# Optimization experiments

Measured on AMD Instinct MI355X. Metric: run time of the kernel, lower is better.

## Reference

```python
import jax, jax.numpy as jnp
import numpy as np

D_MODEL = 1024
NUM_HEADS = 16
HEAD_DIM = D_MODEL // NUM_HEADS


def setup_inputs() -> dict:
    key = jax.random.key(0)
    ks = jax.random.split(key, 11)
    B, S = 2, 2048
    s = 1.0 / np.sqrt(D_MODEL)
    return {
        "q": jax.random.normal(ks[0], (B, S, D_MODEL), jnp.float32),
        "k": jax.random.normal(ks[1], (B, S, D_MODEL), jnp.float32),
        "v": jax.random.normal(ks[2], (B, S, D_MODEL), jnp.float32),
        "Wq": jax.random.normal(ks[3], (D_MODEL, D_MODEL), jnp.float32) * s,
        "bq": jnp.zeros((D_MODEL,), jnp.float32),
        "Wk": jax.random.normal(ks[4], (D_MODEL, D_MODEL), jnp.float32) * s,
        "bk": jnp.zeros((D_MODEL,), jnp.float32),
        "Wv": jax.random.normal(ks[5], (D_MODEL, D_MODEL), jnp.float32) * s,
        "bv": jnp.zeros((D_MODEL,), jnp.float32),
        "Wo": jax.random.normal(ks[6], (D_MODEL, D_MODEL), jnp.float32) * s,
        "bo": jnp.zeros((D_MODEL,), jnp.float32),
    }


def _split_heads(x):
    B, S, _ = x.shape
    return x.reshape(B, S, NUM_HEADS, HEAD_DIM).transpose(0, 2, 1, 3)  # [B,H,S,Dh]


def reference(q, k, v, Wq, bq, Wk, bk, Wv, bv, Wo, bo):
    B, S, _ = q.shape
    qh = _split_heads(q @ Wq.T + bq)
    kh = _split_heads(k @ Wk.T + bk)
    vh = _split_heads(v @ Wv.T + bv)
    scale = 1.0 / jnp.sqrt(jnp.asarray(HEAD_DIM, qh.dtype))
    scores = jnp.einsum("bhqd,bhkd->bhqk", qh, kh) * scale  # [B,H,S,S]
    attn = jax.nn.softmax(scores, axis=-1)
    out = jnp.einsum("bhqk,bhkd->bhqd", attn, vh)
    out = out.transpose(0, 2, 1, 3).reshape(B, S, D_MODEL)
    return out @ Wo.T + bo
```

## Files before the change

### kernel.cpp

```cpp
#include <hip/hip_runtime.h>
#include <cstdint>
#include <cstddef>

#define DEVI __device__ __forceinline__

typedef short bf16x8 __attribute__((ext_vector_type(8)));
typedef float f32x4 __attribute__((ext_vector_type(4)));
typedef unsigned short u16x4 __attribute__((ext_vector_type(4)));

constexpr int D_MODEL = 1024;
constexpr int HEADS = 16;
constexpr int DH = 64;
constexpr int SEQ = 2048;
constexpr int KDIM = 1024;

DEVI unsigned short f2bf(float f) {
  union { float f; unsigned u; } v; v.f = f;
  unsigned r = v.u + 0x7fffu + ((v.u >> 16) & 1u);
  return (unsigned short)(r >> 16);
}

DEVI void cp16(const void* g, void* l) {
  __builtin_amdgcn_global_load_lds(
      (const __attribute__((address_space(1))) void*)g,
      (__attribute__((address_space(3))) void*)l, 16, 0, 0);
}

__global__ void __launch_bounds__(256) castall(
    const float* __restrict__ q, const float* __restrict__ k, const float* __restrict__ v,
    const float* __restrict__ Wq, const float* __restrict__ Wk,
    const float* __restrict__ Wv, const float* __restrict__ Wo,
    unsigned short* __restrict__ qb, unsigned short* __restrict__ kb, unsigned short* __restrict__ vb,
    unsigned short* __restrict__ Wqb, unsigned short* __restrict__ Wkb,
    unsigned short* __restrict__ Wvb, unsigned short* __restrict__ Wob) {
  int bid = blockIdx.x;
  const float* s; unsigned short* d; int off;
  if (bid < 12288) {
    int w = bid >> 12; off = bid & 4095;
    s = (w == 0) ? q : ((w == 1) ? k : v);
    d = (w == 0) ? qb : ((w == 1) ? kb : vb);
  } else {
    int w = (bid - 12288) >> 10; off = bid & 1023;
    s = (w == 0) ? Wq : ((w == 1) ? Wk : ((w == 2) ? Wv : Wo));
    d = (w == 0) ? Wqb : ((w == 1) ? Wkb : ((w == 2) ? Wvb : Wob));
  }
  int i = (off * 256 + threadIdx.x) * 4;
  float4 x = *(const float4*)(s + i);
  u16x4 o; o[0] = f2bf(x.x); o[1] = f2bf(x.y); o[2] = f2bf(x.z); o[3] = f2bf(x.w);
  *(u16x4*)(d + i) = o;
}

DEVI void gemm_body(const unsigned short* __restrict__ A, const unsigned short* __restrict__ W,
                    const float* __restrict__ bias, unsigned short* __restrict__ obf,
                    float* __restrict__ of32, float oscale, int mode, int bm, int bn,
                    unsigned short* As, unsigned short* Bs) {
  const int tid = threadIdx.x, lane = tid & 63, wave = tid >> 6;
  const int l16 = lane & 15, quad = lane >> 4;
  const int wm = (wave >> 1) * 64, wn = (wave & 1) * 64;
  const int sw = (l16 >> 1) & 3;
  f32x4 acc[4][4] = {};

  for (int k0 = 0; k0 < KDIM; k0 += 32) {
#pragma unroll
    for (int c = 0; c < 2; ++c) {
      int slot = c * 256 + tid;
      int row = slot >> 2, pblk = slot & 3;
      int col = (pblk ^ ((row >> 1) & 3)) * 8;
      cp16(A + (size_t)(bm * 128 + row) * KDIM + k0 + col, &As[slot * 8]);
      cp16(W + (size_t)(bn * 128 + row) * KDIM + k0 + col, &Bs[slot * 8]);
    }
    asm volatile("s_waitcnt vmcnt(0)" ::: "memory");
    __syncthreads();
    bf16x8 af[4], bfr[4];
#pragma unroll
    for (int t = 0; t < 4; ++t)
      af[t] = *(const bf16x8*)&As[(wm + t * 16 + l16) * 32 + ((quad ^ sw) * 8)];
#pragma unroll
    for (int t = 0; t < 4; ++t)
      bfr[t] = *(const bf16x8*)&Bs[(wn + t * 16 + l16) * 32 + ((quad ^ sw) * 8)];
#pragma unroll
    for (int i = 0; i < 4; ++i)
#pragma unroll
      for (int j = 0; j < 4; ++j)
        acc[i][j] = __builtin_amdgcn_mfma_f32_16x16x32_bf16(af[i], bfr[j], acc[i][j], 0, 0, 0);
    __syncthreads();
  }

#pragma unroll
  for (int i = 0; i < 4; ++i) {
#pragma unroll
    for (int j = 0; j < 4; ++j) {
      const int col = bn * 128 + wn + j * 16 + l16;
      const float bv = bias[col];
#pragma unroll
      for (int r = 0; r < 4; ++r) {
        const int row = bm * 128 + wm + i * 16 + quad * 4 + r;
        const float val = (acc[i][j][r] + bv) * oscale;
        if (mode == 2) {
          of32[(size_t)row * D_MODEL + col] = val;
        } else {
          const int b = row >> 11, s = row & (SEQ - 1);
          const int h = col >> 6, d = col & (DH - 1);
          size_t idx;
          if (mode == 0) idx = ((size_t)(b * HEADS + h) * SEQ + s) * DH + d;
          else           idx = ((size_t)(b * HEADS + h) * DH + d) * SEQ + s;
          obf[idx] = f2bf(val);
        }
      }
    }
  }
}

__global__ void __launch_bounds__(256) qkv_gemm(
    const unsigned short* __restrict__ qb, const unsigned short* __restrict__ kb,
    const unsigned short* __restrict__ vb,
    const unsigned short* __restrict__ Wqb, const unsigned short* __restrict__ Wkb,
    const unsigned short* __restrict__ Wvb,
    const float* __restrict__ bq, const float* __restrict__ bk, const float* __restrict__ bv,
    unsigned short* __restrict__ Qh, unsigned short* __restrict__ Kh,
    unsigned short* __restrict__ Vt, float qscale) {
  __shared__ unsigned short As[128 * 32], Bs[128 * 32];
  const int bid = blockIdx.x, seg = bid >> 8, inner = bid & 255;
  const int bm = inner >> 3, bn = inner & 7;
  const unsigned short* A = (seg == 0) ? qb : ((seg == 1) ? kb : vb);
  const unsigned short* W = (seg == 0) ? Wqb : ((seg == 1) ? Wkb : Wvb);
  const float* bias = (seg == 0) ? bq : ((seg == 1) ? bk : bv);
  unsigned short* O = (seg == 0) ? Qh : ((seg == 1) ? Kh : Vt);
  gemm_body(A, W, bias, O, nullptr, (seg == 0) ? qscale : 1.0f, (seg == 2) ? 1 : 0, bm, bn, As, Bs);
}

__global__ void __launch_bounds__(256) out_gemm(const unsigned short* __restrict__ AO,
                                                const unsigned short* __restrict__ Wob,
                                                const float* __restrict__ bo,
                                                float* __restrict__ out) {
  __shared__ unsigned short As[128 * 32], Bs[128 * 32];
  const int bid = blockIdx.x, bm = bid >> 3, bn = bid & 7;
  gemm_body(AO, Wob, bo, nullptr, out, 1.0f, 2, bm, bn, As, Bs);
}

__global__ void __launch_bounds__(256) attn(const unsigned short* __restrict__ Qh,
                                            const unsigned short* __restrict__ Kh,
                                            const unsigned short* __restrict__ Vt,
                                            unsigned short* __restrict__ AO) {
  __shared__ unsigned short Ks[2 * 64 * 64];
  __shared__ unsigned short Vs[2 * 64 * 64];
  __shared__ unsigned short Ps[4][16 * 64];
  const int bid = blockIdx.x;
  const int qt = bid >> 5, head = bid & 31, b = head >> 4, h = head & 15;
  const int tid = threadIdx.x;
  const int lane = tid & 63, wave = tid >> 6;
  const int l16 = lane & 15, quad = lane >> 4;
  const int sw7 = l16 & 7;

  const unsigned short* Qhead = Qh + (size_t)(b * HEADS + h) * SEQ * DH;
  const unsigned short* Khead = Kh + (size_t)(b * HEADS + h) * SEQ * DH;
  const unsigned short* Vhead = Vt + (size_t)(b * HEADS + h) * DH * SEQ;

  const int qrow = qt * 64 + wave * 16 + l16;
  bf16x8 aq0 = *(const bf16x8*)&Qhead[(size_t)qrow * DH + quad * 8];
  bf16x8 aq1 = *(const bf16x8*)&Qhead[(size_t)qrow * DH + 32 + quad * 8];

  const short onev = (l16 == 0) ? (short)0x3F80 : (short)0;
  bf16x8 bone = {onev, onev, onev, onev, onev, onev, onev, onev};

  f32x4 o[4] = {};
  f32x4 ol = {};

  for (int kc = 0; kc < SEQ / 128; ++kc) {
    const unsigned short* Kc = Khead + (size_t)kc * 128 * DH;
#pragma unroll
    for (int c = 0; c < 4; ++c) {
      int slot = c * 256 + tid;
      int row = slot >> 3;
      int jb = (slot & 7) ^ (row & 7);
      cp16(Kc + (size_t)row * DH + jb * 8, &Ks[slot * 8]);
      int sub = slot >> 9, s512 = slot & 511;
      int d = s512 >> 3;
      int jv = (s512 & 7) ^ (d & 7);
      cp16(Vhead + (size_t)d * SEQ + kc * 128 + sub * 64 + jv * 8, &Vs[slot * 8]);
    }
    asm volatile("s_waitcnt vmcnt(0)" ::: "memory");
    __syncthreads();

#pragma unroll
    for (int sub = 0; sub < 2; ++sub) {
      const unsigned short* K64 = &Ks[sub * 4096];
      const unsigned short* V64 = &Vs[sub * 4096];

      f32x4 st[4];
#pragma unroll
      for (int kt = 0; kt < 4; ++kt) {
        const int krow = kt * 16 + l16;
        bf16x8 bk0 = *(const bf16x8*)&K64[krow * 64 + ((quad ^ sw7) * 8)];
        bf16x8 bk1 = *(const bf16x8*)&K64[krow * 64 + (((quad + 4) ^ sw7) * 8)];
        f32x4 z = {};
        z = __builtin_amdgcn_mfma_f32_16x16x32_bf16(aq0, bk0, z, 0, 0, 0);
        z = __builtin_amdgcn_mfma_f32_16x16x32_bf16(aq1, bk1, z, 0, 0, 0);
        st[kt] = z;
      }

#pragma unroll
      for (int kt = 0; kt < 4; ++kt) {
        const int lb = kt * 2 + (l16 >> 3);
#pragma unroll
        for (int r = 0; r < 4; ++r) {
          const int rr = quad * 4 + r;
          float p = __builtin_amdgcn_exp2f(st[kt][r]);
          Ps[wave][rr * 64 + ((lb ^ (rr & 7)) << 3) + (l16 & 7)] =
              (unsigned short)(__float_as_uint(p) >> 16);
        }
      }
      asm volatile("s_waitcnt lgkmcnt(0)" ::: "memory");

      bf16x8 ap0 = *(const bf16x8*)&Ps[wave][l16 * 64 + ((quad ^ sw7) << 3)];
      bf16x8 ap1 = *(const bf16x8*)&Ps[wave][l16 * 64 + (((quad + 4) ^ sw7) << 3)];
#pragma unroll
      for (int nt = 0; nt < 4; ++nt) {
        const int vrow = nt * 16 + l16;
        bf16x8 bv0 = *(const bf16x8*)&V64[vrow * 64 + ((quad ^ sw7) * 8)];
        bf16x8 bv1 = *(const bf16x8*)&V64[vrow * 64 + (((quad + 4) ^ sw7) * 8)];
        o[nt] = __builtin_amdgcn_mfma_f32_16x16x32_bf16(ap0, bv0, o[nt], 0, 0, 0);
        o[nt] = __builtin_amdgcn_mfma_f32_16x16x32_bf16(ap1, bv1, o[nt], 0, 0, 0);
      }
      ol = __builtin_amdgcn_mfma_f32_16x16x32_bf16(ap0, bone, ol, 0, 0, 0);
      ol = __builtin_amdgcn_mfma_f32_16x16x32_bf16(ap1, bone, ol, 0, 0, 0);
    }
    __syncthreads();
  }

  float linv[4];
#pragma unroll
  for (int r = 0; r < 4; ++r) {
    float l = __shfl(ol[r], 0, 16);
    linv[r] = 1.0f / l;
  }
#pragma unroll
  for (int nt = 0; nt < 4; ++nt)
#pragma unroll
    for (int r = 0; r < 4; ++r) {
      const int qq = qt * 64 + wave * 16 + quad * 4 + r;
      AO[((size_t)(b * SEQ + qq)) * D_MODEL + h * 64 + nt * 16 + l16] =
          f2bf(o[nt][r] * linv[r]);
    }
}

extern "C" void kernel_launch(void* const* d_in, const int* in_sizes, int n_in,
                              void* d_out, int out_size, void* d_ws, size_t ws_size,
                              hipStream_t stream) {
  const float* q  = (const float*)d_in[0];
  const float* k  = (const float*)d_in[1];
  const float* v  = (const float*)d_in[2];
  const float* Wq = (const float*)d_in[3];
  const float* bq = (const float*)d_in[4];
  const float* Wk = (const float*)d_in[5];
  const float* bk = (const float*)d_in[6];
  const float* Wv = (const float*)d_in[7];
  const float* bv = (const float*)d_in[8];
  const float* Wo = (const float*)d_in[9];
  const float* bo = (const float*)d_in[10];
  float* out = (float*)d_out;

  char* ws = (char*)d_ws;
  const size_t MB = 1ull << 20;
  unsigned short* qb  = (unsigned short*)(ws + 0 * MB);
  unsigned short* kb  = (unsigned short*)(ws + 8 * MB);
  unsigned short* vb  = (unsigned short*)(ws + 16 * MB);
  unsigned short* Wqb = (unsigned short*)(ws + 24 * MB);
  unsigned short* Wkb = (unsigned short*)(ws + 26 * MB);
  unsigned short* Wvb = (unsigned short*)(ws + 28 * MB);
  unsigned short* Wob = (unsigned short*)(ws + 30 * MB);
  unsigned short* Qh  = (unsigned short*)(ws + 32 * MB);
  unsigned short* Kh  = (unsigned short*)(ws + 40 * MB);
  unsigned short* Vt  = (unsigned short*)(ws + 48 * MB);
  unsigned short* AO  = (unsigned short*)(ws + 56 * MB);

  castall<<<16384, 256, 0, stream>>>(q, k, v, Wq, Wk, Wv, Wo,
                                     qb, kb, vb, Wqb, Wkb, Wvb, Wob);

  const float qscale = 0.125f * 1.44269504088896f;
  qkv_gemm<<<768, 256, 0, stream>>>(qb, kb, vb, Wqb, Wkb, Wvb, bq, bk, bv,
                                    Qh, Kh, Vt, qscale);

  attn<<<1024, 256, 0, stream>>>(Qh, Kh, Vt, AO);

  out_gemm<<<256, 256, 0, stream>>>(AO, Wob, bo, out);
}
```

Before: 244.2 us.

## Use 32x32 MFMA register-resident attention and 64-row GEMM tiles

The attention kernel is rebuilt around 32x32 MFMA tiles. Scores are computed transposed so the exponentiated probabilities stay in registers as the B operand of the PV product, which removes the per-wave LDS round trip for P. The row sum is kept as a scalar instead of an extra MFMA, and the two key-split waves are reduced through LDS with a coalesced epilogue store. The projection GEMMs also move from 128x128 to 64x128 tiles, doubling the grid to raise occupancy at the cost of more reloads of the weight tiles.

```diff
diff --git a/kernel.cpp b/kernel.cpp
--- a/kernel.cpp
+++ b/kernel.cpp
@@ -5,7 +5,9 @@
 #define DEVI __device__ __forceinline__
 
 typedef short bf16x8 __attribute__((ext_vector_type(8)));
+typedef short bf16x4 __attribute__((ext_vector_type(4)));
 typedef float f32x4 __attribute__((ext_vector_type(4)));
+typedef float f32x16 __attribute__((ext_vector_type(16)));
 typedef unsigned short u16x4 __attribute__((ext_vector_type(4)));
 
 constexpr int D_MODEL = 1024;
@@ -20,10 +22,23 @@
   return (unsigned short)(r >> 16);
 }
 
+DEVI unsigned pkbf(float a, float b) {
+  return __builtin_amdgcn_perm(__float_as_uint(b), __float_as_uint(a), 0x07060302u);
+}
+
 DEVI void cp16(const void* g, void* l) {
   __builtin_amdgcn_global_load_lds(
       (const __attribute__((address_space(1))) void*)g,
       (__attribute__((address_space(3))) void*)l, 16, 0, 0);
+}
+
+DEVI f32x16 mfma_32x32x8(bf16x4 a, bf16x4 b, f32x16 c) {
+#if __has_builtin(__builtin_amdgcn_mfma_f32_32x32x8bf16_1k)
+  return __builtin_amdgcn_mfma_f32_32x32x8bf16_1k(a, b, c, 0, 0, 0);
+#else
+  asm volatile("v_mfma_f32_32x32x8_bf16 %0, %1, %2, %0" : "+v"(c) : "v"(a), "v"(b));
+  return c;
+#endif
 }
 
 __global__ void __launch_bounds__(256) castall(
@@ -50,38 +65,42 @@
   *(u16x4*)(d + i) = o;
 }
 
-DEVI void gemm_body(const unsigned short* __restrict__ A, const unsigned short* __restrict__ W,
-                    const float* __restrict__ bias, unsigned short* __restrict__ obf,
-                    float* __restrict__ of32, float oscale, int mode, int bm, int bn,
-                    unsigned short* As, unsigned short* Bs) {
+DEVI void gemm_body64(const unsigned short* __restrict__ A, const unsigned short* __restrict__ W,
+                      const float* __restrict__ bias, unsigned short* __restrict__ obf,
+                      float* __restrict__ of32, float oscale, int mode, int bm, int bn,
+                      unsigned short* As, unsigned short* Bs) {
   const int tid = threadIdx.x, lane = tid & 63, wave = tid >> 6;
   const int l16 = lane & 15, quad = lane >> 4;
-  const int wm = (wave >> 1) * 64, wn = (wave & 1) * 64;
+  const int wn = wave * 32;
   const int sw = (l16 >> 1) & 3;
-  f32x4 acc[4][4] = {};
+  f32x4 acc[4][2] = {};
 
   for (int k0 = 0; k0 < KDIM; k0 += 32) {
+    {
+      int row = tid >> 2, pblk = tid & 3;
+      int col = (pblk ^ ((row >> 1) & 3)) * 8;
+      cp16(A + (size_t)(bm * 64 + row) * KDIM + k0 + col, &As[tid * 8]);
+    }
 #pragma unroll
     for (int c = 0; c < 2; ++c) {
       int slot = c * 256 + tid;
       int row = slot >> 2, pblk = slot & 3;
       int col = (pblk ^ ((row >> 1) & 3)) * 8;
-      cp16(A + (size_t)(bm * 128 + row) * KDIM + k0 + col, &As[slot * 8]);
       cp16(W + (size_t)(bn * 128 + row) * KDIM + k0 + col, &Bs[slot * 8]);
     }
     asm volatile("s_waitcnt vmcnt(0)" ::: "memory");
     __syncthreads();
-    bf16x8 af[4], bfr[4];
+    bf16x8 af[4], bfr[2];
 #pragma unroll
     for (int t = 0; t < 4; ++t)
-      af[t] = *(const bf16x8*)&As[(wm + t * 16 + l16) * 32 + ((quad ^ sw) * 8)];
-#pragma unroll
-    for (int t = 0; t < 4; ++t)
-      bfr[t] = *(const bf16x8*)&Bs[(wn + t * 16 + l16) * 32 + ((quad ^ sw) * 8)];
+      af[t] = *(const bf16x8*)&As[(t * 16 + l16) * 32 + ((quad ^ sw) * 8)];
+#pragma unroll
+    for (int u = 0; u < 2; ++u)
+      bfr[u] = *(const bf16x8*)&Bs[(wn + u * 16 + l16) * 32 + ((quad ^ sw) * 8)];
 #pragma unroll
     for (int i = 0; i < 4; ++i)
 #pragma unroll
-      for (int j = 0; j < 4; ++j)
+      for (int j = 0; j < 2; ++j)
         acc[i][j] = __builtin_amdgcn_mfma_f32_16x16x32_bf16(af[i], bfr[j], acc[i][j], 0, 0, 0);
     __syncthreads();
   }
@@ -89,12 +108,12 @@
 #pragma unroll
   for (int i = 0; i < 4; ++i) {
 #pragma unroll
-    for (int j = 0; j < 4; ++j) {
+    for (int j = 0; j < 2; ++j) {
       const int col = bn * 128 + wn + j * 16 + l16;
       const float bv = bias[col];
 #pragma unroll
       for (int r = 0; r < 4; ++r) {
-        const int row = bm * 128 + wm + i * 16 + quad * 4 + r;
+        const int row = bm * 64 + i * 16 + quad * 4 + r;
         const float val = (acc[i][j][r] + bv) * oscale;
         if (mode == 2) {
           of32[(size_t)row * D_MODEL + col] = val;
@@ -119,129 +138,157 @@
     const float* __restrict__ bq, const float* __restrict__ bk, const float* __restrict__ bv,
     unsigned short* __restrict__ Qh, unsigned short* __restrict__ Kh,
     unsigned short* __restrict__ Vt, float qscale) {
-  __shared__ unsigned short As[128 * 32], Bs[128 * 32];
-  const int bid = blockIdx.x, seg = bid >> 8, inner = bid & 255;
+  __shared__ unsigned short As[64 * 32], Bs[128 * 32];
+  const int bid = blockIdx.x, seg = bid >> 9, inner = bid & 511;
   const int bm = inner >> 3, bn = inner & 7;
   const unsigned short* A = (seg == 0) ? qb : ((seg == 1) ? kb : vb);
   const unsigned short* W = (seg == 0) ? Wqb : ((seg == 1) ? Wkb : Wvb);
   const float* bias = (seg == 0) ? bq : ((seg == 1) ? bk : bv);
   unsigned short* O = (seg == 0) ? Qh : ((seg == 1) ? Kh : Vt);
-  gemm_body(A, W, bias, O, nullptr, (seg == 0) ? qscale : 1.0f, (seg == 2) ? 1 : 0, bm, bn, As, Bs);
+  gemm_body64(A, W, bias, O, nullptr, (seg == 0) ? qscale : 1.0f, (seg == 2) ? 1 : 0, bm, bn, As, Bs);
 }
 
 __global__ void __launch_bounds__(256) out_gemm(const unsigned short* __restrict__ AO,
                                                 const unsigned short* __restrict__ Wob,
                                                 const float* __restrict__ bo,
                                                 float* __restrict__ out) {
-  __shared__ unsigned short As[128 * 32], Bs[128 * 32];
+  __shared__ unsigned short As[64 * 32], Bs[128 * 32];
   const int bid = blockIdx.x, bm = bid >> 3, bn = bid & 7;
-  gemm_body(AO, Wob, bo, nullptr, out, 1.0f, 2, bm, bn, As, Bs);
+  gemm_body64(AO, Wob, bo, nullptr, out, 1.0f, 2, bm, bn, As, Bs);
 }
 
 __global__ void __launch_bounds__(256) attn(const unsigned short* __restrict__ Qh,
                                             const unsigned short* __restrict__ Kh,
                                             const unsigned short* __restrict__ Vt,
                                             unsigned short* __restrict__ AO) {
-  __shared__ unsigned short Ks[2 * 64 * 64];
-  __shared__ unsigned short Vs[2 * 64 * 64];
-  __shared__ unsigned short Ps[4][16 * 64];
+  __shared__ __align__(16) char smem[32768];
+  unsigned short* Ks = (unsigned short*)smem;
+  unsigned short* Vs = (unsigned short*)(smem + 16384);
+
   const int bid = blockIdx.x;
   const int qt = bid >> 5, head = bid & 31, b = head >> 4, h = head & 15;
   const int tid = threadIdx.x;
   const int lane = tid & 63, wave = tid >> 6;
-  const int l16 = lane & 15, quad = lane >> 4;
-  const int sw7 = l16 & 7;
+  const int wq = wave >> 1, wk = wave & 1;
+  const int l31 = lane & 31, hh = lane >> 5;
 
   const unsigned short* Qhead = Qh + (size_t)(b * HEADS + h) * SEQ * DH;
   const unsigned short* Khead = Kh + (size_t)(b * HEADS + h) * SEQ * DH;
   const unsigned short* Vhead = Vt + (size_t)(b * HEADS + h) * DH * SEQ;
 
-  const int qrow = qt * 64 + wave * 16 + l16;
-  bf16x8 aq0 = *(const bf16x8*)&Qhead[(size_t)qrow * DH + quad * 8];
-  bf16x8 aq1 = *(const bf16x8*)&Qhead[(size_t)qrow * DH + 32 + quad * 8];
-
-  const short onev = (l16 == 0) ? (short)0x3F80 : (short)0;
-  bf16x8 bone = {onev, onev, onev, onev, onev, onev, onev, onev};
-
-  f32x4 o[4] = {};
-  f32x4 ol = {};
+  const int qrow = qt * 64 + wq * 32 + l31;
+  bf16x8 aq[4];
+#pragma unroll
+  for (int it = 0; it < 4; ++it)
+    aq[it] = *(const bf16x8*)&Qhead[(size_t)qrow * DH + it * 16 + hh * 8];
+
+  f32x16 oacc[2] = {};
+  float lsum = 0.f;
 
   for (int kc = 0; kc < SEQ / 128; ++kc) {
-    const unsigned short* Kc = Khead + (size_t)kc * 128 * DH;
 #pragma unroll
     for (int c = 0; c < 4; ++c) {
-      int slot = c * 256 + tid;
-      int row = slot >> 3;
-      int jb = (slot & 7) ^ (row & 7);
-      cp16(Kc + (size_t)row * DH + jb * 8, &Ks[slot * 8]);
-      int sub = slot >> 9, s512 = slot & 511;
-      int d = s512 >> 3;
-      int jv = (s512 & 7) ^ (d & 7);
-      cp16(Vhead + (size_t)d * SEQ + kc * 128 + sub * 64 + jv * 8, &Vs[slot * 8]);
+      int s = c * 256 + tid;
+      int row = s >> 3, pblk = s & 7;
+      int jb = pblk ^ (row & 7);
+      cp16(Khead + (size_t)(kc * 128 + row) * DH + jb * 8, &Ks[s * 8]);
+    }
+#pragma unroll
+    for (int c = 0; c < 4; ++c) {
+      int s = c * 256 + tid;
+      int d = s >> 4, pblk = s & 15;
+      int jb = pblk ^ (d & 7);
+      cp16(Vhead + (size_t)d * SEQ + kc * 128 + jb * 8, &Vs[s * 8]);
     }
     asm volatile("s_waitcnt vmcnt(0)" ::: "memory");
     __syncthreads();
 
 #pragma unroll
     for (int sub = 0; sub < 2; ++sub) {
-      const unsigned short* K64 = &Ks[sub * 4096];
-      const unsigned short* V64 = &Vs[sub * 4096];
-
-      f32x4 st[4];
-#pragma unroll
-      for (int kt = 0; kt < 4; ++kt) {
-        const int krow = kt * 16 + l16;
-        bf16x8 bk0 = *(const bf16x8*)&K64[krow * 64 + ((quad ^ sw7) * 8)];
-        bf16x8 bk1 = *(const bf16x8*)&K64[krow * 64 + (((quad + 4) ^ sw7) * 8)];
-        f32x4 z = {};
-        z = __builtin_amdgcn_mfma_f32_16x16x32_bf16(aq0, bk0, z, 0, 0, 0);
-        z = __builtin_amdgcn_mfma_f32_16x16x32_bf16(aq1, bk1, z, 0, 0, 0);
-        st[kt] = z;
-      }
-
-#pragma unroll
-      for (int kt = 0; kt < 4; ++kt) {
-        const int lb = kt * 2 + (l16 >> 3);
-#pragma unroll
-        for (int r = 0; r < 4; ++r) {
-          const int rr = quad * 4 + r;
-          float p = __builtin_amdgcn_exp2f(st[kt][r]);
-          Ps[wave][rr * 64 + ((lb ^ (rr & 7)) << 3) + (l16 & 7)] =
-              (unsigned short)(__float_as_uint(p) >> 16);
+      const int kb32 = sub * 64 + wk * 32;
+      const int key = kb32 + l31;
+
+      f32x16 sa = {};
+#pragma unroll
+      for (int it = 0; it < 4; ++it) {
+        const int sblk = (2 * it + hh) ^ (key & 7);
+        bf16x8 ak = *(const bf16x8*)&Ks[key * 64 + sblk * 8];
+        sa = __builtin_amdgcn_mfma_f32_32x32x16_bf16(ak, aq[it], sa, 0, 0, 0);
+      }
+
+      float p[16];
+#pragma unroll
+      for (int r = 0; r < 16; ++r) {
+        p[r] = __builtin_amdgcn_exp2f(sa[r]);
+        lsum += p[r];
+      }
+      bf16x4 pk[4];
+#pragma unroll
+      for (int g = 0; g < 4; ++g) {
+        union { unsigned u[2]; bf16x4 s; } c;
+        c.u[0] = pkbf(p[4 * g + 0], p[4 * g + 1]);
+        c.u[1] = pkbf(p[4 * g + 2], p[4 * g + 3]);
+        pk[g] = c.s;
+      }
+
+#pragma unroll
+      for (int g = 0; g < 4; ++g) {
+        const int gblk = sub * 8 + wk * 4 + g;
+#pragma unroll
+        for (int dh2 = 0; dh2 < 2; ++dh2) {
+          const int d = dh2 * 32 + l31;
+          const int sv = gblk ^ (d & 7);
+          bf16x4 av = *(const bf16x4*)&Vs[d * 128 + sv * 8 + hh * 4];
+          oacc[dh2] = mfma_32x32x8(av, pk[g], oacc[dh2]);
         }
       }
-      asm volatile("s_waitcnt lgkmcnt(0)" ::: "memory");
-
-      bf16x8 ap0 = *(const bf16x8*)&Ps[wave][l16 * 64 + ((quad ^ sw7) << 3)];
-      bf16x8 ap1 = *(const bf16x8*)&Ps[wave][l16 * 64 + (((quad + 4) ^ sw7) << 3)];
-#pragma unroll
-      for (int nt = 0; nt < 4; ++nt) {
-        const int vrow = nt * 16 + l16;
-        bf16x8 bv0 = *(const bf16x8*)&V64[vrow * 64 + ((quad ^ sw7) * 8)];
-        bf16x8 bv1 = *(const bf16x8*)&V64[vrow * 64 + (((quad + 4) ^ sw7) * 8)];
-        o[nt] = __builtin_amdgcn_mfma_f32_16x16x32_bf16(ap0, bv0, o[nt], 0, 0, 0);
-        o[nt] = __builtin_amdgcn_mfma_f32_16x16x32_bf16(ap1, bv1, o[nt], 0, 0, 0);
-      }
-      ol = __builtin_amdgcn_mfma_f32_16x16x32_bf16(ap0, bone, ol, 0, 0, 0);
-      ol = __builtin_amdgcn_mfma_f32_16x16x32_bf16(ap1, bone, ol, 0, 0, 0);
     }
     __syncthreads();
   }
 
-  float linv[4];
-#pragma unroll
-  for (int r = 0; r < 4; ++r) {
-    float l = __shfl(ol[r], 0, 16);
-    linv[r] = 1.0f / l;
-  }
-#pragma unroll
-  for (int nt = 0; nt < 4; ++nt)
-#pragma unroll
-    for (int r = 0; r < 4; ++r) {
-      const int qq = qt * 64 + wave * 16 + quad * 4 + r;
-      AO[((size_t)(b * SEQ + qq)) * D_MODEL + h * 64 + nt * 16 + l16] =
-          f2bf(o[nt][r] * linv[r]);
-    }
+  lsum += __shfl_xor(lsum, 32);
+
+  float* epiF = (float*)smem;
+  float* lbuf = (float*)(smem + 16384);
+  unsigned short* Oq = (unsigned short*)(smem + 17408);
+
+  if (l31 == lane) lbuf[wave * 32 + l31] = lsum;
+  if (wk == 1) {
+#pragma unroll
+    for (int dh2 = 0; dh2 < 2; ++dh2)
+#pragma unroll
+      for (int r = 0; r < 16; ++r) {
+        const int d = dh2 * 32 + (r & 3) + 8 * (r >> 2) + 4 * hh;
+        epiF[wq * 2048 + d * 32 + l31] = oacc[dh2][r];
+      }
+  }
+  __syncthreads();
+
+  if (wk == 0) {
+    const float linv = 1.0f / (lsum + lbuf[(wq * 2 + 1) * 32 + l31]);
+#pragma unroll
+    for (int dh2 = 0; dh2 < 2; ++dh2) {
+#pragma unroll
+      for (int r = 0; r < 16; r += 2) {
+        const int d = dh2 * 32 + (r & 3) + 8 * (r >> 2) + 4 * hh;
+        const float v0 = (oacc[dh2][r]     + epiF[wq * 2048 + d * 32 + l31]) * linv;
+        const float v1 = (oacc[dh2][r + 1] + epiF[wq * 2048 + (d + 1) * 32 + l31]) * linv;
+        *(unsigned*)&Oq[wq * 2176 + l31 * 68 + d] = pkbf(v0, v1);
+      }
+    }
+  }
+  __syncthreads();
+
+  {
+    const int qloc = tid >> 2, d0 = (tid & 3) * 16;
+    const int base = (qloc >> 5) * 2176 + (qloc & 31) * 68 + d0;
+    unsigned u[8];
+#pragma unroll
+    for (int i = 0; i < 8; ++i) u[i] = *(const unsigned*)&Oq[base + i * 2];
+    unsigned short* dst = AO + ((size_t)(b * SEQ + qt * 64 + qloc)) * D_MODEL + h * 64 + d0;
+    *(uint4*)dst       = make_uint4(u[0], u[1], u[2], u[3]);
+    *(uint4*)(dst + 8) = make_uint4(u[4], u[5], u[6], u[7]);
+  }
 }
 
 extern "C" void kernel_launch(void* const* d_in, const int* in_sizes, int n_in,
@@ -278,10 +325,10 @@
                                      qb, kb, vb, Wqb, Wkb, Wvb, Wob);
 
   const float qscale = 0.125f * 1.44269504088896f;
-  qkv_gemm<<<768, 256, 0, stream>>>(qb, kb, vb, Wqb, Wkb, Wvb, bq, bk, bv,
-                                    Qh, Kh, Vt, qscale);
+  qkv_gemm<<<1536, 256, 0, stream>>>(qb, kb, vb, Wqb, Wkb, Wvb, bq, bk, bv,
+                                     Qh, Kh, Vt, qscale);
 
   attn<<<1024, 256, 0, stream>>>(Qh, Kh, Vt, AO);
 
-  out_gemm<<<256, 256, 0, stream>>>(AO, Wob, bo, out);
-}
+  out_gemm<<<512, 256, 0, stream>>>(AO, Wob, bo, out);
+}
```

After: 253.2 us. 3.7% more time.
